# Optimization experiments

Hardware: AMD Instinct MI355X
Metric: run time of the kernel (lower is better)

## Reference

```python
import jax, jax.numpy as jnp
import numpy as np

N_MICS = 8
REF_MIC = 0
DIAG_LOAD = 1e-5
PI_ITERS = 30  # power-iteration steps for principal eigenvector of Phi_nn^-1 Phi_ss


def setup_inputs() -> dict:
    key = jax.random.key(0)
    k1, k2, k3, k4 = jax.random.split(key, 4)
    B, M, F, T = 8, N_MICS, 257, 2000
    return {
        "spec_re": jax.random.normal(k1, (B, M, F, T), dtype=jnp.float32),
        "spec_im": jax.random.normal(k2, (B, M, F, T), dtype=jnp.float32),
        "speech_mask": jax.random.uniform(k3, (B, F, T), dtype=jnp.float32),
        "noise_mask": jax.random.uniform(k4, (B, F, T), dtype=jnp.float32),
    }


def _mvdr(spec_re, spec_im, speech_mask, noise_mask):
    # (B, M, F, T) complex STFT -> (B, F, M, T) for per-(batch, freq) processing
    Y = (spec_re + 1j * spec_im).astype(jnp.complex64)
    Y = jnp.transpose(Y, (0, 2, 1, 3))  # (B, F, M, T)
    M = Y.shape[2]

    def masked_cov(mask):  # mask: (B, F, T) real
        msum = mask.sum(-1) + 1e-8                       # (B, F)
        Yw = Y * mask[:, :, None, :]                      # (B, F, M, T)
        Phi = jnp.einsum('bfmt,bfnt->bfmn', Yw, Y.conj())  # (B, F, M, M)
        return Phi / msum[..., None, None]

    Phi_ss = masked_cov(speech_mask)
    eye = jnp.eye(M, dtype=jnp.complex64)
    Phi_nn = masked_cov(noise_mask) + DIAG_LOAD * eye

    Phi_nn_inv = jnp.linalg.inv(Phi_nn)                   # batched (B, F, M, M)
    G = jnp.einsum('bfmn,bfnk->bfmk', Phi_nn_inv, Phi_ss)

    # Principal eigenvector of G via power iteration (G has real, nonnegative
    # eigenvalues since it is similar to a Hermitian-PSD generalized pencil),
    # matching torch.linalg.eig + argmax(eigenvalues.real) up to scale.
    v = jnp.ones(G.shape[:-1], dtype=jnp.complex64)       # (B, F, M)
    for _ in range(PI_ITERS):
        v = jnp.einsum('bfmn,bfn->bfm', G, v)
        v = v / (jnp.linalg.norm(v, axis=-1, keepdims=True) + 1e-12)

    # Relative transfer function normalized to reference mic (removes scale)
    rtf = v / (v[..., REF_MIC:REF_MIC + 1] + 1e-8)        # (B, F, M)

    d = jnp.einsum('bfmn,bfn->bfm', Phi_nn_inv, rtf)      # Phi_nn^-1 rtf
    denom = jnp.einsum('bfm,bfm->bf', rtf.conj(), d).real + 1e-8
    w = d / denom[..., None]                              # (B, F, M) MVDR weights

    enhanced = jnp.einsum('bfm,bfmt->bft', w.conj(), Y)   # (B, F, T) complex
    return enhanced


def reference(spec_re, spec_im, speech_mask, noise_mask):
    return _mvdr(spec_re, spec_im, speech_mask, noise_mask)
```

## Files before the change

### kernel.cpp

```cpp
#include <hip/hip_runtime.h>

#define B_DIM 8
#define M_MICS 8
#define F_DIM 257
#define T_DIM 2000
#define NPROB (B_DIM * F_DIM)

__device__ float g_w[NPROB * 16];


#define PAIR_ACC(a, bb, k)                                              \
    {                                                                   \
        const float pr = yr[a][u] * yr[bb][u] + yi[a][u] * yi[bb][u];   \
        const float pi = yi[a][u] * yr[bb][u] - yr[a][u] * yi[bb][u];   \
        acc[(k) + 0] += msv[u] * pr;                                    \
        acc[(k) + 1] += msv[u] * pi;                                    \
        acc[(k) + 2] += mnv[u] * pr;                                    \
        acc[(k) + 3] += mnv[u] * pi;                                    \
    }

#define LOAD4(k, m)                                                                                 \
    {                                                                                               \
        const float4 vr_ = *reinterpret_cast<const float4*>(sre + base_bf + (size_t)(m) * mrow + t0); \
        const float4 vi_ = *reinterpret_cast<const float4*>(sim + base_bf + (size_t)(m) * mrow + t0); \
        yr[k][0] = vr_.x; yr[k][1] = vr_.y; yr[k][2] = vr_.z; yr[k][3] = vr_.w;                     \
        yi[k][0] = vi_.x; yi[k][1] = vi_.y; yi[k][2] = vi_.z; yi[k][3] = vi_.w;                     \
    }

#define MASK4                                                                              \
    const float4 ms4 = *reinterpret_cast<const float4*>(smask + mbase + t0);               \
    const float4 mn4 = *reinterpret_cast<const float4*>(nmask + mbase + t0);               \
    const float msv[4] = { ms4.x, ms4.y, ms4.z, ms4.w };                                   \
    const float mnv[4] = { mn4.x, mn4.y, mn4.z, mn4.w };

#define PAIR_LOOP(BODY_LOADS, BODY_ACCS, KMICS)                         \
    {                                                                   \
        _Pragma("unroll 1")                                             \
        for (int it = 0; it < 8; ++it) {                                \
            const int t0 = 4 * l + 256 * it;                            \
            if (t0 < T_DIM) {                                           \
                float yr[KMICS][4], yi[KMICS][4];                       \
                BODY_LOADS                                              \
                MASK4                                                   \
                _Pragma("unroll")                                       \
                for (int u = 0; u < 4; ++u) { BODY_ACCS }               \
            }                                                           \
        }                                                               \
    }

__launch_bounds__(512, 4)
__global__ void cov_solve_kernel(const float* __restrict__ sre, const float* __restrict__ sim,
                                 const float* __restrict__ smask, const float* __restrict__ nmask)
{
    const int f = blockIdx.x, b = blockIdx.y, tid = threadIdx.x;
    const int h = tid >> 6, l = tid & 63;

    __shared__ float sG[8][20];

    const size_t mrow = (size_t)F_DIM * T_DIM;
    const size_t base_bf = ((size_t)(b * M_MICS) * F_DIM + f) * T_DIM;
    const size_t mbase   = ((size_t)b * F_DIM + f) * T_DIM;

    float acc[18];
#pragma unroll
    for (int i = 0; i < 18; ++i) acc[i] = 0.f;

    if (h == 0) {
#pragma unroll 1
        for (int it = 0; it < 16; ++it) {
            const int t0 = 2 * l + 128 * it;
            if (t0 < T_DIM) {
                float yr[8][2], yi[8][2];
#pragma unroll
                for (int m = 0; m < 8; ++m) {
                    const float2 vr_ = *reinterpret_cast<const float2*>(sre + base_bf + (size_t)m * mrow + t0);
                    const float2 vi_ = *reinterpret_cast<const float2*>(sim + base_bf + (size_t)m * mrow + t0);
                    yr[m][0] = vr_.x; yr[m][1] = vr_.y;
                    yi[m][0] = vi_.x; yi[m][1] = vi_.y;
                }
                const float2 ms2 = *reinterpret_cast<const float2*>(smask + mbase + t0);
                const float2 mn2 = *reinterpret_cast<const float2*>(nmask + mbase + t0);
                const float msv[2] = { ms2.x, ms2.y };
                const float mnv[2] = { mn2.x, mn2.y };
#pragma unroll
                for (int u = 0; u < 2; ++u) {
                    acc[0] += msv[u];
                    acc[1] += mnv[u];
#pragma unroll
                    for (int m = 0; m < 8; ++m) {
                        const float pd = yr[m][u] * yr[m][u] + yi[m][u] * yi[m][u];
                        acc[2 + m]  += msv[u] * pd;
                        acc[10 + m] += mnv[u] * pd;
                    }
                }
            }
        }
    } else if (h == 1) {
        PAIR_LOOP(LOAD4(0,0) LOAD4(1,1) LOAD4(2,2) LOAD4(3,3) LOAD4(4,4),
                  PAIR_ACC(0,1,0) PAIR_ACC(0,2,4) PAIR_ACC(0,3,8) PAIR_ACC(0,4,12), 5)
    } else if (h == 2) {
        PAIR_LOOP(LOAD4(0,0) LOAD4(1,1) LOAD4(2,2) LOAD4(3,5) LOAD4(4,6) LOAD4(5,7),
                  PAIR_ACC(0,3,0) PAIR_ACC(0,4,4) PAIR_ACC(0,5,8) PAIR_ACC(1,2,12), 6)
    } else if (h == 3) {
        PAIR_LOOP(LOAD4(0,1) LOAD4(1,3) LOAD4(2,4) LOAD4(3,5) LOAD4(4,6),
                  PAIR_ACC(0,1,0) PAIR_ACC(0,2,4) PAIR_ACC(0,3,8) PAIR_ACC(0,4,12), 5)
    } else if (h == 4) {
        PAIR_LOOP(LOAD4(0,1) LOAD4(1,2) LOAD4(2,3) LOAD4(3,4) LOAD4(4,5) LOAD4(5,7),
                  PAIR_ACC(0,5,0) PAIR_ACC(1,2,4) PAIR_ACC(1,3,8) PAIR_ACC(1,4,12), 6)
    } else if (h == 5) {
        PAIR_LOOP(LOAD4(0,2) LOAD4(1,3) LOAD4(2,4) LOAD4(3,5) LOAD4(4,6) LOAD4(5,7),
                  PAIR_ACC(0,4,0) PAIR_ACC(0,5,4) PAIR_ACC(1,2,8) PAIR_ACC(1,3,12), 6)
    } else if (h == 6) {
        PAIR_LOOP(LOAD4(0,3) LOAD4(1,4) LOAD4(2,5) LOAD4(3,6) LOAD4(4,7),
                  PAIR_ACC(0,3,0) PAIR_ACC(0,4,4) PAIR_ACC(1,2,8) PAIR_ACC(1,3,12), 5)
    } else {
        PAIR_LOOP(LOAD4(0,4) LOAD4(1,5) LOAD4(2,6) LOAD4(3,7),
                  PAIR_ACC(0,3,0) PAIR_ACC(1,2,4) PAIR_ACC(1,3,8) PAIR_ACC(2,3,12), 4)
    }

#pragma unroll
    for (int i = 0; i < 18; ++i) {
        acc[i] += __shfl_xor(acc[i], 1, 64);
        acc[i] += __shfl_xor(acc[i], 2, 64);
        acc[i] += __shfl_xor(acc[i], 4, 64);
        acc[i] += __shfl_xor(acc[i], 8, 64);
        acc[i] += __shfl_xor(acc[i], 16, 64);
        acc[i] += __shfl_xor(acc[i], 32, 64);
    }
    if (l == 0) {
#pragma unroll
        for (int i = 0; i < 18; ++i) sG[h][i] = acc[i];
    }
    __syncthreads();

    if (tid < 64) {
        const int r = tid >> 3, cc = tid & 7;
        const float Ssum = sG[0][0] + 1e-8f;
        const float Nsum = sG[0][1] + 1e-8f;

        float ssr, ssi, ar, ai;
        if (r == cc) {
            ssr = sG[0][2 + r] / Ssum;  ssi = 0.f;
            ar  = sG[0][10 + r] / Nsum + 1e-5f;  ai = 0.f;
        } else {
            const int mm  = (r < cc) ? r : cc;
            const int nn2 = (r < cc) ? cc : r;
            const int q = mm * 8 - mm * (mm + 1) / 2 + nn2 - mm - 1;
            const int g = 1 + (q >> 2);
            const int basei = 4 * (q & 3);
            const float sgn = (r < cc) ? 1.f : -1.f;
            ssr = sG[g][basei] / Ssum;
            ssi = sgn * sG[g][basei + 1] / Ssum;
            ar  = sG[g][basei + 2] / Nsum;
            ai  = sgn * sG[g][basei + 3] / Nsum;
        }

        float br = (r == cc) ? 1.f : 0.f, bi = 0.f;
        for (int k = 0; k < 8; ++k) {
            const float pr = __shfl(ar, k * 9, 64);
            const float pi = __shfl(ai, k * 9, 64);
            const float den = pr * pr + pi * pi;
            const float qr = pr / den, qi = -pi / den;
            const bool isk = (r == k);
            const float ar2 = ar * qr - ai * qi;
            const float ai2 = ar * qi + ai * qr;
            const float br2 = br * qr - bi * qi;
            const float bi2 = br * qi + bi * qr;
            ar = isk ? ar2 : ar; ai = isk ? ai2 : ai;
            br = isk ? br2 : br; bi = isk ? bi2 : bi;
            const float rar = __shfl(ar, k * 8 + cc, 64);
            const float rai = __shfl(ai, k * 8 + cc, 64);
            const float rbr = __shfl(br, k * 8 + cc, 64);
            const float rbi = __shfl(bi, k * 8 + cc, 64);
            const float fr = __shfl(ar, r * 8 + k, 64);
            const float fi = __shfl(ai, r * 8 + k, 64);
            const float uar = ar - (fr * rar - fi * rai);
            const float uai = ai - (fr * rai + fi * rar);
            const float ubr = br - (fr * rbr - fi * rbi);
            const float ubi = bi - (fr * rbi + fi * rbr);
            ar = isk ? ar : uar; ai = isk ? ai : uai;
            br = isk ? br : ubr; bi = isk ? bi : ubi;
        }

        float gr = 0.f, gi = 0.f;
        for (int k = 0; k < 8; ++k) {
            const float ir = __shfl(br, r * 8 + k, 64);
            const float ii = __shfl(bi, r * 8 + k, 64);
            const float skr = __shfl(ssr, k * 8 + cc, 64);
            const float ski = __shfl(ssi, k * 8 + cc, 64);
            gr += ir * skr - ii * ski;
            gi += ir * ski + ii * skr;
        }

        float vr = 1.f, vi = 0.f;
        for (int itp = 0; itp < 30; ++itp) {
            float wr2 = gr * vr - gi * vi;
            float wi2 = gr * vi + gi * vr;
            wr2 += __shfl_xor(wr2, 1, 64); wi2 += __shfl_xor(wi2, 1, 64);
            wr2 += __shfl_xor(wr2, 2, 64); wi2 += __shfl_xor(wi2, 2, 64);
            wr2 += __shfl_xor(wr2, 4, 64); wi2 += __shfl_xor(wi2, 4, 64);
            float nrm = wr2 * wr2 + wi2 * wi2;
            nrm += __shfl_xor(nrm, 8, 64);
            nrm += __shfl_xor(nrm, 16, 64);
            nrm += __shfl_xor(nrm, 32, 64);
            const float inv = 1.f / (sqrtf(nrm) + 1e-12f);
            wr2 *= inv; wi2 *= inv;
            vr = __shfl(wr2, cc * 9, 64);
            vi = __shfl(wi2, cc * 9, 64);
        }

        const float v0r = __shfl(vr, 0, 64) + 1e-8f;
        const float v0i = __shfl(vi, 0, 64);
        const float dd = v0r * v0r + v0i * v0i;
        const float rtr = (vr * v0r + vi * v0i) / dd;
        const float rti = (vi * v0r - vr * v0i) / dd;

        float dr = br * rtr - bi * rti;
        float di = br * rti + bi * rtr;
        dr += __shfl_xor(dr, 1, 64); di += __shfl_xor(di, 1, 64);
        dr += __shfl_xor(dr, 2, 64); di += __shfl_xor(di, 2, 64);
        dr += __shfl_xor(dr, 4, 64); di += __shfl_xor(di, 4, 64);

        float qden = (r == cc) ? (rtr * dr + rti * di) : 0.f;
        qden += __shfl_xor(qden, 1, 64); qden += __shfl_xor(qden, 2, 64);
        qden += __shfl_xor(qden, 4, 64); qden += __shfl_xor(qden, 8, 64);
        qden += __shfl_xor(qden, 16, 64); qden += __shfl_xor(qden, 32, 64);
        qden += 1e-8f;

        if (cc == 0) {
            const int p = b * F_DIM + f;
            g_w[p * 16 + r]     = dr / qden;
            g_w[p * 16 + 8 + r] = di / qden;
        }
    }
}

__launch_bounds__(256, 8)
__global__ void apply_kernel(const float* __restrict__ sre, const float* __restrict__ sim,
                             float* __restrict__ out, int out_mode)
{
    const int f = blockIdx.x, b = blockIdx.y, z = blockIdx.z;
    const int tid = threadIdx.x;
    __shared__ float sW[16];
    const int p = b * F_DIM + f;
    if (tid < 16) sW[tid] = g_w[p * 16 + tid];
    __syncthreads();

    const int t0 = z * 512 + 2 * tid;
    if (t0 >= T_DIM) return;

    const size_t mrow = (size_t)F_DIM * T_DIM;
    const size_t base_bf = ((size_t)(b * M_MICS) * F_DIM + f) * T_DIM;
    const size_t mbase   = ((size_t)b * F_DIM + f) * T_DIM;

    float er0 = 0.f, ei0 = 0.f, er1 = 0.f, ei1 = 0.f;
#pragma unroll
    for (int m = 0; m < 8; ++m) {
        const float2 vr2 = *reinterpret_cast<const float2*>(sre + base_bf + (size_t)m * mrow + t0);
        const float2 vi2 = *reinterpret_cast<const float2*>(sim + base_bf + (size_t)m * mrow + t0);
        const float wr = sW[m], wi = sW[8 + m];
        er0 += wr * vr2.x + wi * vi2.x;
        ei0 += wr * vi2.x - wi * vr2.x;
        er1 += wr * vr2.y + wi * vi2.y;
        ei1 += wr * vi2.y - wi * vr2.y;
    }
    if (out_mode == 2) {
        *reinterpret_cast<float4*>(out + 2 * (mbase + t0)) = make_float4(er0, ei0, er1, ei1);
    } else {
        *reinterpret_cast<float2*>(out + mbase + t0) = make_float2(er0, er1);
    }
}

extern "C" void kernel_launch(void* const* d_in, const int* in_sizes, int n_in,
                              void* d_out, int out_size, void* d_ws, size_t ws_size,
                              hipStream_t stream)
{
    const float* sre   = (const float*)d_in[0];
    const float* sim   = (const float*)d_in[1];
    const float* smask = (const float*)d_in[2];
    const float* nmask = (const float*)d_in[3];
    float* out = (float*)d_out;

    const int mode = (out_size >= 2 * B_DIM * F_DIM * T_DIM) ? 2 : 1;

    cov_solve_kernel<<<dim3(F_DIM, B_DIM), 512, 0, stream>>>(sre, sim, smask, nmask);
    apply_kernel<<<dim3(F_DIM, B_DIM, 4), 256, 0, stream>>>(sre, sim, out, mode);
}
```

Before: 174.3 us.

## Stage mic and mask tiles into LDS with double-buffered async global loads

Each wave now loads only its own mic's real and imaginary rows, plus one mask, into a shared LDS tile using global_load_lds. Loads run into a double buffer while the current tile is computed. All waves then read their 4–6 mic rows from LDS instead of re-reading them from global memory. This removes the redundant global and L2 reads of each mic row across waves, and overlaps loading with compute. In exchange it adds about 37 KB of LDS per block, which may limit occupancy, and one block-wide barrier per tile.

Result: slower. 178.4 us (+2.3%).

```diff
diff --git a/kernel.cpp b/kernel.cpp
--- a/kernel.cpp
+++ b/kernel.cpp
@@ -5,8 +5,15 @@
 #define F_DIM 257
 #define T_DIM 2000
 #define NPROB (B_DIM * F_DIM)
+#define TILE 256
+#define NFULL 7
+#define TAILW 208
 
 __device__ float g_w[NPROB * 16];
+
+#define GLOAD_LDS(g, s) __builtin_amdgcn_global_load_lds(                       \
+    (const __attribute__((address_space(1))) void*)(g),                         \
+    (__attribute__((address_space(3))) void*)(s), 16, 0, 0)
 
 
 #define PAIR_ACC(a, bb, k)                                              \
@@ -19,33 +26,20 @@
         acc[(k) + 3] += mnv[u] * pi;                                    \
     }
 
-#define LOAD4(k, m)                                                                                 \
-    {                                                                                               \
-        const float4 vr_ = *reinterpret_cast<const float4*>(sre + base_bf + (size_t)(m) * mrow + t0); \
-        const float4 vi_ = *reinterpret_cast<const float4*>(sim + base_bf + (size_t)(m) * mrow + t0); \
-        yr[k][0] = vr_.x; yr[k][1] = vr_.y; yr[k][2] = vr_.z; yr[k][3] = vr_.w;                     \
-        yi[k][0] = vi_.x; yi[k][1] = vi_.y; yi[k][2] = vi_.z; yi[k][3] = vi_.w;                     \
-    }
-
-#define MASK4                                                                              \
-    const float4 ms4 = *reinterpret_cast<const float4*>(smask + mbase + t0);               \
-    const float4 mn4 = *reinterpret_cast<const float4*>(nmask + mbase + t0);               \
-    const float msv[4] = { ms4.x, ms4.y, ms4.z, ms4.w };                                   \
-    const float mnv[4] = { mn4.x, mn4.y, mn4.z, mn4.w };
-
-#define PAIR_LOOP(BODY_LOADS, BODY_ACCS, KMICS)                         \
+#define LOADM(k, mic)                                                             \
+    {                                                                             \
+        const float4 vr_ = *reinterpret_cast<const float4*>(&lds[bb][mic][4 * l]);      \
+        const float4 vi_ = *reinterpret_cast<const float4*>(&lds[bb][8 + (mic)][4 * l]);\
+        yr[k][0] = vr_.x; yr[k][1] = vr_.y; yr[k][2] = vr_.z; yr[k][3] = vr_.w;   \
+        yi[k][0] = vi_.x; yi[k][1] = vi_.y; yi[k][2] = vi_.z; yi[k][3] = vi_.w;   \
+    }
+
+#define PAIR_BODY(LOADS, ACCS, KM)                                      \
     {                                                                   \
-        _Pragma("unroll 1")                                             \
-        for (int it = 0; it < 8; ++it) {                                \
-            const int t0 = 4 * l + 256 * it;                            \
-            if (t0 < T_DIM) {                                           \
-                float yr[KMICS][4], yi[KMICS][4];                       \
-                BODY_LOADS                                              \
-                MASK4                                                   \
-                _Pragma("unroll")                                       \
-                for (int u = 0; u < 4; ++u) { BODY_ACCS }               \
-            }                                                           \
-        }                                                               \
+        float yr[KM][4], yi[KM][4];                                     \
+        LOADS                                                           \
+        _Pragma("unroll")                                               \
+        for (int u = 0; u < 4; ++u) { ACCS }                            \
     }
 
 __launch_bounds__(512, 4)
@@ -55,67 +49,94 @@
     const int f = blockIdx.x, b = blockIdx.y, tid = threadIdx.x;
     const int h = tid >> 6, l = tid & 63;
 
+    __shared__ float lds[2][18][TILE];
     __shared__ float sG[8][20];
 
     const size_t mrow = (size_t)F_DIM * T_DIM;
     const size_t base_bf = ((size_t)(b * M_MICS) * F_DIM + f) * T_DIM;
     const size_t mbase   = ((size_t)b * F_DIM + f) * T_DIM;
 
+    const float* g_re = sre + base_bf + (size_t)h * mrow;
+    const float* g_im = sim + base_bf + (size_t)h * mrow;
+    const float* g_ms = smask + mbase;
+    const float* g_mn = nmask + mbase;
+
     float acc[18];
 #pragma unroll
     for (int i = 0; i < 18; ++i) acc[i] = 0.f;
 
-    if (h == 0) {
-#pragma unroll 1
-        for (int it = 0; it < 16; ++it) {
-            const int t0 = 2 * l + 128 * it;
-            if (t0 < T_DIM) {
-                float yr[8][2], yi[8][2];
-#pragma unroll
-                for (int m = 0; m < 8; ++m) {
-                    const float2 vr_ = *reinterpret_cast<const float2*>(sre + base_bf + (size_t)m * mrow + t0);
-                    const float2 vi_ = *reinterpret_cast<const float2*>(sim + base_bf + (size_t)m * mrow + t0);
-                    yr[m][0] = vr_.x; yr[m][1] = vr_.y;
-                    yi[m][0] = vi_.x; yi[m][1] = vi_.y;
-                }
-                const float2 ms2 = *reinterpret_cast<const float2*>(smask + mbase + t0);
-                const float2 mn2 = *reinterpret_cast<const float2*>(nmask + mbase + t0);
-                const float msv[2] = { ms2.x, ms2.y };
-                const float mnv[2] = { mn2.x, mn2.y };
-#pragma unroll
-                for (int u = 0; u < 2; ++u) {
-                    acc[0] += msv[u];
-                    acc[1] += mnv[u];
-#pragma unroll
-                    for (int m = 0; m < 8; ++m) {
-                        const float pd = yr[m][u] * yr[m][u] + yi[m][u] * yi[m][u];
-                        acc[2 + m]  += msv[u] * pd;
-                        acc[10 + m] += mnv[u] * pd;
-                    }
+    auto STAGE = [&](int bb, int toff, int tw) {
+        if (4 * l < tw) {
+            GLOAD_LDS(g_re + toff + 4 * l, &lds[bb][h][0]);
+            GLOAD_LDS(g_im + toff + 4 * l, &lds[bb][8 + h][0]);
+            if (h == 0)      GLOAD_LDS(g_ms + toff + 4 * l, &lds[bb][16][0]);
+            else if (h == 1) GLOAD_LDS(g_mn + toff + 4 * l, &lds[bb][17][0]);
+        }
+    };
+
+    auto COMPUTE = [&](int bb) {
+        float msv[4], mnv[4];
+        {
+            const float4 v = *reinterpret_cast<const float4*>(&lds[bb][16][4 * l]);
+            msv[0] = v.x; msv[1] = v.y; msv[2] = v.z; msv[3] = v.w;
+        }
+        {
+            const float4 v = *reinterpret_cast<const float4*>(&lds[bb][17][4 * l]);
+            mnv[0] = v.x; mnv[1] = v.y; mnv[2] = v.z; mnv[3] = v.w;
+        }
+        if (h == 0) {
+            acc[0] += msv[0] + msv[1] + msv[2] + msv[3];
+            acc[1] += mnv[0] + mnv[1] + mnv[2] + mnv[3];
+#pragma unroll
+            for (int m = 0; m < 8; ++m) {
+                const float4 re4 = *reinterpret_cast<const float4*>(&lds[bb][m][4 * l]);
+                const float4 im4 = *reinterpret_cast<const float4*>(&lds[bb][8 + m][4 * l]);
+                const float rr[4] = { re4.x, re4.y, re4.z, re4.w };
+                const float ii[4] = { im4.x, im4.y, im4.z, im4.w };
+#pragma unroll
+                for (int u = 0; u < 4; ++u) {
+                    const float pd = rr[u] * rr[u] + ii[u] * ii[u];
+                    acc[2 + m]  += msv[u] * pd;
+                    acc[10 + m] += mnv[u] * pd;
                 }
             }
-        }
-    } else if (h == 1) {
-        PAIR_LOOP(LOAD4(0,0) LOAD4(1,1) LOAD4(2,2) LOAD4(3,3) LOAD4(4,4),
-                  PAIR_ACC(0,1,0) PAIR_ACC(0,2,4) PAIR_ACC(0,3,8) PAIR_ACC(0,4,12), 5)
-    } else if (h == 2) {
-        PAIR_LOOP(LOAD4(0,0) LOAD4(1,1) LOAD4(2,2) LOAD4(3,5) LOAD4(4,6) LOAD4(5,7),
-                  PAIR_ACC(0,3,0) PAIR_ACC(0,4,4) PAIR_ACC(0,5,8) PAIR_ACC(1,2,12), 6)
-    } else if (h == 3) {
-        PAIR_LOOP(LOAD4(0,1) LOAD4(1,3) LOAD4(2,4) LOAD4(3,5) LOAD4(4,6),
-                  PAIR_ACC(0,1,0) PAIR_ACC(0,2,4) PAIR_ACC(0,3,8) PAIR_ACC(0,4,12), 5)
-    } else if (h == 4) {
-        PAIR_LOOP(LOAD4(0,1) LOAD4(1,2) LOAD4(2,3) LOAD4(3,4) LOAD4(4,5) LOAD4(5,7),
-                  PAIR_ACC(0,5,0) PAIR_ACC(1,2,4) PAIR_ACC(1,3,8) PAIR_ACC(1,4,12), 6)
-    } else if (h == 5) {
-        PAIR_LOOP(LOAD4(0,2) LOAD4(1,3) LOAD4(2,4) LOAD4(3,5) LOAD4(4,6) LOAD4(5,7),
-                  PAIR_ACC(0,4,0) PAIR_ACC(0,5,4) PAIR_ACC(1,2,8) PAIR_ACC(1,3,12), 6)
-    } else if (h == 6) {
-        PAIR_LOOP(LOAD4(0,3) LOAD4(1,4) LOAD4(2,5) LOAD4(3,6) LOAD4(4,7),
-                  PAIR_ACC(0,3,0) PAIR_ACC(0,4,4) PAIR_ACC(1,2,8) PAIR_ACC(1,3,12), 5)
-    } else {
-        PAIR_LOOP(LOAD4(0,4) LOAD4(1,5) LOAD4(2,6) LOAD4(3,7),
-                  PAIR_ACC(0,3,0) PAIR_ACC(1,2,4) PAIR_ACC(1,3,8) PAIR_ACC(2,3,12), 4)
+        } else if (h == 1) {
+            PAIR_BODY(LOADM(0,0) LOADM(1,1) LOADM(2,2) LOADM(3,3) LOADM(4,4),
+                      PAIR_ACC(0,1,0) PAIR_ACC(0,2,4) PAIR_ACC(0,3,8) PAIR_ACC(0,4,12), 5)
+        } else if (h == 2) {
+            PAIR_BODY(LOADM(0,0) LOADM(1,1) LOADM(2,2) LOADM(3,5) LOADM(4,6) LOADM(5,7),
+                      PAIR_ACC(0,3,0) PAIR_ACC(0,4,4) PAIR_ACC(0,5,8) PAIR_ACC(1,2,12), 6)
+        } else if (h == 3) {
+            PAIR_BODY(LOADM(0,1) LOADM(1,3) LOADM(2,4) LOADM(3,5) LOADM(4,6),
+                      PAIR_ACC(0,1,0) PAIR_ACC(0,2,4) PAIR_ACC(0,3,8) PAIR_ACC(0,4,12), 5)
+        } else if (h == 4) {
+            PAIR_BODY(LOADM(0,1) LOADM(1,2) LOADM(2,3) LOADM(3,4) LOADM(4,5) LOADM(5,7),
+                      PAIR_ACC(0,5,0) PAIR_ACC(1,2,4) PAIR_ACC(1,3,8) PAIR_ACC(1,4,12), 6)
+        } else if (h == 5) {
+            PAIR_BODY(LOADM(0,2) LOADM(1,3) LOADM(2,4) LOADM(3,5) LOADM(4,6) LOADM(5,7),
+                      PAIR_ACC(0,4,0) PAIR_ACC(0,5,4) PAIR_ACC(1,2,8) PAIR_ACC(1,3,12), 6)
+        } else if (h == 6) {
+            PAIR_BODY(LOADM(0,3) LOADM(1,4) LOADM(2,5) LOADM(3,6) LOADM(4,7),
+                      PAIR_ACC(0,3,0) PAIR_ACC(0,4,4) PAIR_ACC(1,2,8) PAIR_ACC(1,3,12), 5)
+        } else {
+            PAIR_BODY(LOADM(0,4) LOADM(1,5) LOADM(2,6) LOADM(3,7),
+                      PAIR_ACC(0,3,0) PAIR_ACC(1,2,4) PAIR_ACC(1,3,8) PAIR_ACC(2,3,12), 4)
+        }
+    };
+
+    STAGE(0, 0, TILE);
+    __syncthreads();
+#pragma unroll 1
+    for (int t = 0; t < NFULL; ++t) {
+        if (t < NFULL - 1) STAGE((t + 1) & 1, (t + 1) * TILE, TILE);
+        else               STAGE(1, NFULL * TILE, TAILW);
+        const int bb = t & 1;
+        COMPUTE(bb);
+        __syncthreads();
+    }
+    if (4 * l < TAILW) {
+        const int bb = 1;
+        COMPUTE(bb);
     }
 
 #pragma unroll
```
